# Optimization experiments

Hardware: AMD Instinct MI355X
Metric: run time of the kernel (lower is better)

Reference implementation:

```python
import jax, jax.numpy as jnp
import numpy as np

B, C, H, W = 32, 384, 28, 28
E, HID, K = 4, 384, 2  # HID = hidden_features(1536) // num_experts(4)


def setup_inputs() -> dict:
    key = jax.random.key(0)
    ks = jax.random.split(key, 5)
    x = jax.random.normal(ks[0], (B, C, H, W), jnp.float32)
    gate_w = jax.random.normal(ks[1], (C, E), jnp.float32) * 0.02
    gate_b = jnp.zeros((E,), jnp.float32)
    w1 = jax.random.normal(ks[2], (E, HID, C), jnp.float32) * 0.02
    b1 = jnp.zeros((E, HID), jnp.float32)
    w2 = jax.random.normal(ks[3], (E, C, HID), jnp.float32) * 0.02
    b2 = jnp.zeros((E, C), jnp.float32)
    return {"x": x, "gate_w": gate_w, "gate_b": gate_b,
            "w1": w1, "b1": b1, "w2": w2, "b2": b2}


def reference(x, gate_w, gate_b, w1, b1, w2, b2):
    b, c, h, w = x.shape
    e = gate_b.shape[0]
    # per-token gating: tokens are spatial positions in NHWC order
    x_flat = x.transpose(0, 2, 3, 1).reshape(-1, c)          # [N, C], N = B*H*W
    scores = jax.nn.softmax(x_flat @ gate_w + gate_b, -1)    # [N, E]
    top_v, top_i = jax.lax.top_k(scores, K)                  # [N, K]
    top_w = jax.nn.softmax(top_v, -1)                        # [N, K] renormalized
    # weight map per top-k slot: [K, B, H, W]
    wmap = top_w.T.reshape(K, b, h, w)
    # faithful to torch loop: expert i contributes at slot k iff ANY token routed
    # to it at slot k; the weight applied is the UNMASKED slot-k weight map.
    present = (top_i[:, :, None] == jnp.arange(e)[None, None, :]).any(0)  # [K, E]
    coef = jnp.einsum('ke,kbhw->ebhw', present.astype(x.dtype), wmap)     # [E, B, H, W]
    # dense per-expert 1x1-conv MLP over the FULL tensor (as in the source)
    hdn = jax.nn.relu(jnp.einsum('bchw,edc->ebdhw', x, w1)
                      + b1[:, None, :, None, None])          # [E, B, HID, H, W]
    y = jnp.einsum('ebdhw,eod->ebohw', hdn, w2) + b2[:, None, :, None, None]
    out = jnp.einsum('ebohw,ebhw->bohw', y, coef)            # [B, C, H, W]
    return out
```

## Files before the change

kernel.cpp:

```cpp
#include <hip/hip_runtime.h>
#include <hip/hip_bf16.h>
#include <stdint.h>

#define B_DIM 32
#define C_DIM 384
#define HW_DIM 784
#define E_DIM 4
#define HID_DIM 384
#define NTOK (B_DIM * HW_DIM)
#define NH (E_DIM * HID_DIM)

using short8 = __attribute__((ext_vector_type(8))) short;
using f32x4  = __attribute__((ext_vector_type(4))) float;
typedef unsigned short ushort_t;

__device__ __forceinline__ ushort_t f2bf(float f) {
  __hip_bfloat16 h = __float2bfloat16(f);
  return __builtin_bit_cast(ushort_t, h);
}

__device__ __forceinline__ void gload_lds16(const void* g, void* l) {
  __builtin_amdgcn_global_load_lds(
      (const __attribute__((address_space(1))) unsigned int*)g,
      (__attribute__((address_space(3))) unsigned int*)l, 16, 0, 0);
}

__global__ __launch_bounds__(256) void prep_kernel(
    const float* __restrict__ w1, const float* __restrict__ w2,
    ushort_t* __restrict__ W1b, ushort_t* __restrict__ W2b,
    unsigned int* __restrict__ present) {
  int i = blockIdx.x * 256 + threadIdx.x;
  if (i == 0) *present = 0u;
  if (i < NH * C_DIM) {
    W1b[i] = f2bf(w1[i]);
    int o = i / NH;
    int r = i - o * NH;
    int e = r / HID_DIM;
    int k = r - e * HID_DIM;
    W2b[i] = f2bf(w2[((size_t)e * C_DIM + o) * HID_DIM + k]);
  }
}

__global__ __launch_bounds__(512) void gate_kernel(
    const float* __restrict__ x, const float* __restrict__ gw,
    const float* __restrict__ gb, ushort_t* __restrict__ xb,
    float* __restrict__ topw, unsigned int* __restrict__ present) {
  __shared__ __align__(16) ushort_t lxs[64][392];
  __shared__ float pscore[8][64][4];
  __shared__ unsigned int pmask;
  const int b = blockIdx.x;
  const int p0 = blockIdx.y * 64;
  const int cnt = min(64, HW_DIM - p0);
  const int tid = threadIdx.x;
  const int cg = tid >> 6, tl = tid & 63;
  if (tid == 0) pmask = 0u;
  float a0 = 0.f, a1 = 0.f, a2 = 0.f, a3 = 0.f;
  const bool valid = tl < cnt;
  if (valid) {
    const float* xp = x + (size_t)b * C_DIM * HW_DIM + p0 + tl;
    for (int c = cg; c < C_DIM; c += 8) {
      const float v = xp[(size_t)c * HW_DIM];
      lxs[tl][c] = f2bf(v);
      const float4 g = *(const float4*)&gw[c * 4];
      a0 += v * g.x; a1 += v * g.y; a2 += v * g.z; a3 += v * g.w;
    }
  }
  pscore[cg][tl][0] = a0; pscore[cg][tl][1] = a1;
  pscore[cg][tl][2] = a2; pscore[cg][tl][3] = a3;
  __syncthreads();
  if (cg == 0 && valid) {
    float z[4];
#pragma unroll
    for (int e = 0; e < 4; e++) {
      float s = gb[e];
#pragma unroll
      for (int g8 = 0; g8 < 8; g8++) s += pscore[g8][tl][e];
      z[e] = s;
    }
    const float mx = fmaxf(fmaxf(z[0], z[1]), fmaxf(z[2], z[3]));
    float s[4]; float sum = 0.f;
#pragma unroll
    for (int e = 0; e < 4; e++) { s[e] = __expf(z[e] - mx); sum += s[e]; }
    const float inv = 1.f / sum;
#pragma unroll
    for (int e = 0; e < 4; e++) s[e] *= inv;
    int e0 = 0; float v0 = s[0];
#pragma unroll
    for (int e = 1; e < 4; e++) if (s[e] > v0) { v0 = s[e]; e0 = e; }
    int e1 = -1; float v1 = -1.f;
#pragma unroll
    for (int e = 0; e < 4; e++) if (e != e0 && s[e] > v1) { v1 = s[e]; e1 = e; }
    const float r = __expf(v1 - v0);
    const float w0 = 1.f / (1.f + r);
    const int m = b * HW_DIM + p0 + tl;
    topw[m * 2] = w0;
    topw[m * 2 + 1] = 1.f - w0;
    atomicOr(&pmask, (1u << e0) | (1u << (4 + e1)));
  }
  __syncthreads();
  if (tid == 0) atomicOr(present, pmask);
  const int nchunk = cnt * 48;
  for (int ci = tid; ci < nchunk; ci += 512) {
    const int row = ci / 48, c8 = ci - row * 48;
    short8 v = *(const short8*)&lxs[row][c8 * 8];
    *(short8*)&xb[(size_t)(b * HW_DIM + p0 + row) * C_DIM + c8 * 8] = v;
  }
}

template <int KDIM, int EPI>
__global__ __launch_bounds__(256, 3) void gemm_1b(
    const ushort_t* __restrict__ A, const ushort_t* __restrict__ Bw,
    const float* __restrict__ bias, const float* __restrict__ topw,
    const unsigned int* __restrict__ presentp,
    ushort_t* __restrict__ hOut, float* __restrict__ outp) {
  constexpr int BM = 128, BN = 128, BK = 32;
  constexpr int KT = KDIM / BK;
  constexpr int NTN = (EPI == 0 ? NH / BN : C_DIM / BN);
  constexpr int ASZ = BM * BK;
  __shared__ ushort_t smem[6 * ASZ];

  const int nwg = NTN * (NTOK / BM);
  const int orig = blockIdx.x;
  const int xcd = orig & 7;
  const int qq = nwg >> 3, rr = nwg & 7;
  const int wg = (xcd < rr ? xcd * (qq + 1) : rr * (qq + 1) + (xcd - rr) * qq)
               + (orig >> 3);
  const int mt = wg / NTN, nt = wg % NTN;
  const int m0 = mt * BM, n0 = nt * BN;

  const int tid = threadIdx.x;
  const int lane = tid & 63;
  const int wid = tid >> 6;
  const int wm = wid >> 1, wn = wid & 1;
  const int lanel = lane & 15, laneq = lane >> 4;

  auto stage = [&](int t) {
    const int buf = t % 3;
    ushort_t* dstA = smem + buf * ASZ;
    ushort_t* dstB = smem + 3 * ASZ + buf * ASZ;
    const int kb = t * BK;
#pragma unroll
    for (int li = 0; li < 2; ++li) {
      const int P = (li * 256 + tid) * 16;
      const int row = P >> 6;
      const int cb = (P & 63) ^ (((row >> 1) & 3) << 4);
      gload_lds16(&A[(size_t)(m0 + row) * KDIM + kb + (cb >> 1)],
                  (char*)dstA + P);
    }
#pragma unroll
    for (int li = 0; li < 2; ++li) {
      const int P = (li * 256 + tid) * 16;
      const int row = P >> 6;
      const int cb = (P & 63) ^ (((row >> 1) & 3) << 4);
      gload_lds16(&Bw[(size_t)(n0 + row) * KDIM + kb + (cb >> 1)],
                  (char*)dstB + P);
    }
  };

  f32x4 acc[4][4] = {};
  const int cbr = (laneq * 16) ^ (((lanel >> 1) & 3) << 4);

  stage(0);
  stage(1);
  for (int t = 0; t < KT; ++t) {
    if (t + 1 < KT)
      asm volatile("s_waitcnt vmcnt(4)" ::: "memory");
    else
      asm volatile("s_waitcnt vmcnt(0)" ::: "memory");
    __builtin_amdgcn_sched_barrier(0);
    __builtin_amdgcn_s_barrier();
    __builtin_amdgcn_sched_barrier(0);
    if (t + 2 < KT) stage(t + 2);
    const int buf = t % 3;
    const char* Ab = (const char*)(smem + buf * ASZ) + (wm * 64 + lanel) * 64;
    const char* Bb =
        (const char*)(smem + 3 * ASZ + buf * ASZ) + (wn * 64 + lanel) * 64;
    short8 av[4], bv[4];
#pragma unroll
    for (int i = 0; i < 4; ++i) av[i] = *(const short8*)(Ab + i * 1024 + cbr);
#pragma unroll
    for (int j = 0; j < 4; ++j) bv[j] = *(const short8*)(Bb + j * 1024 + cbr);
    __builtin_amdgcn_s_setprio(1);
#pragma unroll
    for (int i = 0; i < 4; ++i)
#pragma unroll
      for (int j = 0; j < 4; ++j)
        acc[i][j] = __builtin_amdgcn_mfma_f32_16x16x32_bf16(
            av[i], bv[j], acc[i][j], 0, 0, 0);
    __builtin_amdgcn_s_setprio(0);
  }

  const unsigned int pm = *presentp;
  if constexpr (EPI == 0) {
    __syncthreads();
    ushort_t* tr = smem;
    const int e = n0 / HID_DIM;
    const float P0 = (float)((pm >> e) & 1u);
    const float P1 = (float)((pm >> (4 + e)) & 1u);
#pragma unroll
    for (int mi = 0; mi < 4; ++mi) {
      const int r0 = wm * 64 + mi * 16 + laneq * 4;
      const int mg = m0 + r0;
      const float4 t0 = *(const float4*)&topw[mg * 2];
      const float4 t1 = *(const float4*)&topw[mg * 2 + 4];
      const float cj[4] = {P0 * t0.x + P1 * t0.y, P0 * t0.z + P1 * t0.w,
                           P0 * t1.x + P1 * t1.y, P0 * t1.z + P1 * t1.w};
#pragma unroll
      for (int ni = 0; ni < 4; ++ni) {
        const int cl = wn * 64 + ni * 16 + lanel;
        const float bvv = bias[n0 + cl];
#pragma unroll
        for (int j = 0; j < 4; ++j) {
          float v = fmaxf(acc[mi][ni][j] + bvv, 0.f);
          tr[(r0 + j) * 128 + cl] = f2bf(cj[j] * v);
        }
      }
    }
    __syncthreads();
#pragma unroll
    for (int it = 0; it < 8; ++it) {
      const int c = it * 256 + tid;
      const int row = c >> 4, cr = c & 15;
      *(short8*)&hOut[(size_t)(m0 + row) * NH + n0 + cr * 8] =
          *(const short8*)&tr[row * 128 + cr * 8];
    }
  } else {
    float B0[4], B1[4];
#pragma unroll
    for (int ni = 0; ni < 4; ++ni) {
      const int o = n0 + wn * 64 + ni * 16 + lanel;
      float s0 = 0.f, s1 = 0.f;
#pragma unroll
      for (int e2 = 0; e2 < 4; ++e2) {
        const float bb = bias[e2 * C_DIM + o];
        s0 += (float)((pm >> e2) & 1u) * bb;
        s1 += (float)((pm >> (4 + e2)) & 1u) * bb;
      }
      B0[ni] = s0; B1[ni] = s1;
    }
#pragma unroll
    for (int mi = 0; mi < 4; ++mi) {
      const int mg = m0 + wm * 64 + mi * 16 + laneq * 4;
      const float4 t0 = *(const float4*)&topw[mg * 2];
      const float4 t1 = *(const float4*)&topw[mg * 2 + 4];
      const int bb2 = mg / HW_DIM;
      const int p = mg - bb2 * HW_DIM;
#pragma unroll
      for (int ni = 0; ni < 4; ++ni) {
        const int o = n0 + wn * 64 + ni * 16 + lanel;
        float4 v;
        v.x = acc[mi][ni][0] + t0.x * B0[ni] + t0.y * B1[ni];
        v.y = acc[mi][ni][1] + t0.z * B0[ni] + t0.w * B1[ni];
        v.z = acc[mi][ni][2] + t1.x * B0[ni] + t1.y * B1[ni];
        v.w = acc[mi][ni][3] + t1.z * B0[ni] + t1.w * B1[ni];
        *(float4*)&outp[((size_t)bb2 * C_DIM + o) * HW_DIM + p] = v;
      }
    }
  }
}

extern "C" void kernel_launch(void* const* d_in, const int* in_sizes, int n_in,
                              void* d_out, int out_size, void* d_ws, size_t ws_size,
                              hipStream_t stream) {
  const float* x  = (const float*)d_in[0];
  const float* gw = (const float*)d_in[1];
  const float* gb = (const float*)d_in[2];
  const float* w1 = (const float*)d_in[3];
  const float* b1 = (const float*)d_in[4];
  const float* w2 = (const float*)d_in[5];
  const float* b2 = (const float*)d_in[6];
  float* out = (float*)d_out;

  char* ws = (char*)d_ws;
  ushort_t* xb = (ushort_t*)ws;   ws += (size_t)NTOK * C_DIM * 2;
  ushort_t* hdnS = (ushort_t*)ws; ws += (size_t)NTOK * NH * 2;
  ushort_t* W1b = (ushort_t*)ws;  ws += (size_t)NH * C_DIM * 2;
  ushort_t* W2b = (ushort_t*)ws;  ws += (size_t)C_DIM * NH * 2;
  float* topw = (float*)ws;       ws += (size_t)NTOK * 2 * 4;
  unsigned int* present = (unsigned int*)ws;

  prep_kernel<<<dim3((NH * C_DIM) / 256), dim3(256), 0, stream>>>(
      w1, w2, W1b, W2b, present);
  gate_kernel<<<dim3(B_DIM, 13), dim3(512), 0, stream>>>(
      x, gw, gb, xb, topw, present);
  gemm_1b<C_DIM, 0>
      <<<dim3((NTOK / 128) * (NH / 128)), dim3(256), 0, stream>>>(
          xb, W1b, b1, topw, present, hdnS, nullptr);
  gemm_1b<NH, 1>
      <<<dim3((NTOK / 128) * (C_DIM / 128)), dim3(256), 0, stream>>>(
          hdnS, W2b, b2, topw, present, nullptr, out);
}
```

Measured before the change: 121.7 us.

## Load pre-swizzled weight fragments directly into registers, bypassing LDS

```diff
diff --git a/kernel.cpp b/kernel.cpp
--- a/kernel.cpp
+++ b/kernel.cpp
@@ -9,6 +9,7 @@
 #define HID_DIM 384
 #define NTOK (B_DIM * HW_DIM)
 #define NH (E_DIM * HID_DIM)
+#define WSZ 589824
 
 using short8 = __attribute__((ext_vector_type(8))) short;
 using f32x4  = __attribute__((ext_vector_type(4))) float;
@@ -27,17 +28,35 @@
 
 __global__ __launch_bounds__(256) void prep_kernel(
     const float* __restrict__ w1, const float* __restrict__ w2,
-    ushort_t* __restrict__ W1b, ushort_t* __restrict__ W2b,
+    ushort_t* __restrict__ W1f, ushort_t* __restrict__ W2f,
     unsigned int* __restrict__ present) {
   int i = blockIdx.x * 256 + threadIdx.x;
   if (i == 0) *present = 0u;
-  if (i < NH * C_DIM) {
-    W1b[i] = f2bf(w1[i]);
-    int o = i / NH;
-    int r = i - o * NH;
-    int e = r / HID_DIM;
-    int k = r - e * HID_DIM;
-    W2b[i] = f2bf(w2[((size_t)e * C_DIM + o) * HID_DIM + k]);
+  if (i >= WSZ) return;
+  {
+    int r = i;
+    const int nt = r / 49152; r -= nt * 49152;
+    const int ks = r / 4096;  r -= ks * 4096;
+    const int wn = r >> 11;
+    const int ni = (r >> 9) & 3;
+    const int ln = (r >> 3) & 63;
+    const int tt = r & 7;
+    const int row = nt * 128 + wn * 64 + ni * 16 + (ln & 15);
+    const int c = ks * 32 + (ln >> 4) * 8 + tt;
+    W1f[i] = f2bf(w1[(size_t)row * C_DIM + c]);
+  }
+  {
+    int r = i;
+    const int nt = r / 196608; r -= nt * 196608;
+    const int ks = r / 4096;   r -= ks * 4096;
+    const int wn = r >> 11;
+    const int ni = (r >> 9) & 3;
+    const int ln = (r >> 3) & 63;
+    const int tt = r & 7;
+    const int o = nt * 128 + wn * 64 + ni * 16 + (ln & 15);
+    const int kg = ks * 32 + (ln >> 4) * 8 + tt;
+    const int e = kg / HID_DIM, d = kg - e * HID_DIM;
+    W2f[i] = f2bf(w2[((size_t)e * C_DIM + o) * HID_DIM + d]);
   }
 }
 
@@ -108,8 +127,8 @@
 }
 
 template <int KDIM, int EPI>
-__global__ __launch_bounds__(256, 3) void gemm_1b(
-    const ushort_t* __restrict__ A, const ushort_t* __restrict__ Bw,
+__global__ __launch_bounds__(256, 3) void gemm_bg(
+    const ushort_t* __restrict__ A, const ushort_t* __restrict__ Wf,
     const float* __restrict__ bias, const float* __restrict__ topw,
     const unsigned int* __restrict__ presentp,
     ushort_t* __restrict__ hOut, float* __restrict__ outp) {
@@ -117,7 +136,7 @@
   constexpr int KT = KDIM / BK;
   constexpr int NTN = (EPI == 0 ? NH / BN : C_DIM / BN);
   constexpr int ASZ = BM * BK;
-  __shared__ ushort_t smem[6 * ASZ];
+  __shared__ ushort_t smem[3 * ASZ];
 
   const int nwg = NTN * (NTOK / BM);
   const int orig = blockIdx.x;
@@ -134,10 +153,10 @@
   const int wm = wid >> 1, wn = wid & 1;
   const int lanel = lane & 15, laneq = lane >> 4;
 
+  const ushort_t* wbase = Wf + (size_t)nt * KT * 4096 + wn * 2048 + lane * 8;
+
   auto stage = [&](int t) {
-    const int buf = t % 3;
-    ushort_t* dstA = smem + buf * ASZ;
-    ushort_t* dstB = smem + 3 * ASZ + buf * ASZ;
+    ushort_t* dstA = smem + (t % 3) * ASZ;
     const int kb = t * BK;
 #pragma unroll
     for (int li = 0; li < 2; ++li) {
@@ -147,47 +166,57 @@
       gload_lds16(&A[(size_t)(m0 + row) * KDIM + kb + (cb >> 1)],
                   (char*)dstA + P);
     }
-#pragma unroll
-    for (int li = 0; li < 2; ++li) {
-      const int P = (li * 256 + tid) * 16;
-      const int row = P >> 6;
-      const int cb = (P & 63) ^ (((row >> 1) & 3) << 4);
-      gload_lds16(&Bw[(size_t)(n0 + row) * KDIM + kb + (cb >> 1)],
-                  (char*)dstB + P);
-    }
+  };
+
+  auto loadB = [&](int t, short8* bv) {
+    const ushort_t* p = wbase + (size_t)t * 4096;
+    asm volatile(
+        "global_load_dwordx4 %0, %4, off\n\t"
+        "global_load_dwordx4 %1, %4, off offset:1024\n\t"
+        "global_load_dwordx4 %2, %4, off offset:2048\n\t"
+        "global_load_dwordx4 %3, %4, off offset:3072"
+        : "=&v"(bv[0]), "=&v"(bv[1]), "=&v"(bv[2]), "=&v"(bv[3])
+        : "v"(p)
+        : "memory");
   };
 
   f32x4 acc[4][4] = {};
   const int cbr = (laneq * 16) ^ (((lanel >> 1) & 3) << 4);
 
-  stage(0);
-  stage(1);
-  for (int t = 0; t < KT; ++t) {
+  short8 bvA[4], bvB[4];
+
+  auto step = [&](int t, short8* cur, short8* nxt) {
     if (t + 1 < KT)
-      asm volatile("s_waitcnt vmcnt(4)" ::: "memory");
+      asm volatile("s_waitcnt vmcnt(2)" ::: "memory");
     else
       asm volatile("s_waitcnt vmcnt(0)" ::: "memory");
     __builtin_amdgcn_sched_barrier(0);
     __builtin_amdgcn_s_barrier();
     __builtin_amdgcn_sched_barrier(0);
+    if (t + 1 < KT) loadB(t + 1, nxt);
+    __builtin_amdgcn_sched_barrier(0);
     if (t + 2 < KT) stage(t + 2);
-    const int buf = t % 3;
-    const char* Ab = (const char*)(smem + buf * ASZ) + (wm * 64 + lanel) * 64;
-    const char* Bb =
-        (const char*)(smem + 3 * ASZ + buf * ASZ) + (wn * 64 + lanel) * 64;
-    short8 av[4], bv[4];
+    const char* Ab =
+        (const char*)(smem + (t % 3) * ASZ) + (wm * 64 + lanel) * 64;
+    short8 av[4];
 #pragma unroll
     for (int i = 0; i < 4; ++i) av[i] = *(const short8*)(Ab + i * 1024 + cbr);
-#pragma unroll
-    for (int j = 0; j < 4; ++j) bv[j] = *(const short8*)(Bb + j * 1024 + cbr);
     __builtin_amdgcn_s_setprio(1);
 #pragma unroll
     for (int i = 0; i < 4; ++i)
 #pragma unroll
       for (int j = 0; j < 4; ++j)
         acc[i][j] = __builtin_amdgcn_mfma_f32_16x16x32_bf16(
-            av[i], bv[j], acc[i][j], 0, 0, 0);
+            av[i], cur[j], acc[i][j], 0, 0, 0);
     __builtin_amdgcn_s_setprio(0);
+  };
+
+  stage(0);
+  loadB(0, bvA);
+  stage(1);
+  for (int t = 0; t < KT; t += 2) {
+    step(t, bvA, bvB);
+    step(t + 1, bvB, bvA);
   }
 
   const unsigned int pm = *presentp;
@@ -198,31 +227,37 @@
     const float P0 = (float)((pm >> e) & 1u);
     const float P1 = (float)((pm >> (4 + e)) & 1u);
 #pragma unroll
-    for (int mi = 0; mi < 4; ++mi) {
-      const int r0 = wm * 64 + mi * 16 + laneq * 4;
-      const int mg = m0 + r0;
-      const float4 t0 = *(const float4*)&topw[mg * 2];
-      const float4 t1 = *(const float4*)&topw[mg * 2 + 4];
-      const float cj[4] = {P0 * t0.x + P1 * t0.y, P0 * t0.z + P1 * t0.w,
-                           P0 * t1.x + P1 * t1.y, P0 * t1.z + P1 * t1.w};
-#pragma unroll
-      for (int ni = 0; ni < 4; ++ni) {
-        const int cl = wn * 64 + ni * 16 + lanel;
-        const float bvv = bias[n0 + cl];
-#pragma unroll
-        for (int j = 0; j < 4; ++j) {
-          float v = fmaxf(acc[mi][ni][j] + bvv, 0.f);
-          tr[(r0 + j) * 128 + cl] = f2bf(cj[j] * v);
+    for (int s = 0; s < 2; ++s) {
+      if (wm == s) {
+#pragma unroll
+        for (int mi = 0; mi < 4; ++mi) {
+          const int r0 = mi * 16 + laneq * 4;
+          const int mg = m0 + s * 64 + r0;
+          const float4 t0 = *(const float4*)&topw[mg * 2];
+          const float4 t1 = *(const float4*)&topw[mg * 2 + 4];
+          const float cj[4] = {P0 * t0.x + P1 * t0.y, P0 * t0.z + P1 * t0.w,
+                               P0 * t1.x + P1 * t1.y, P0 * t1.z + P1 * t1.w};
+#pragma unroll
+          for (int ni = 0; ni < 4; ++ni) {
+            const int cl = wn * 64 + ni * 16 + lanel;
+            const float bvv = bias[n0 + cl];
+#pragma unroll
+            for (int j = 0; j < 4; ++j) {
+              float v = fmaxf(acc[mi][ni][j] + bvv, 0.f);
+              tr[(r0 + j) * 128 + cl] = f2bf(cj[j] * v);
+            }
+          }
         }
       }
-    }
-    __syncthreads();
-#pragma unroll
-    for (int it = 0; it < 8; ++it) {
-      const int c = it * 256 + tid;
-      const int row = c >> 4, cr = c & 15;
-      *(short8*)&hOut[(size_t)(m0 + row) * NH + n0 + cr * 8] =
-          *(const short8*)&tr[row * 128 + cr * 8];
+      __syncthreads();
+#pragma unroll
+      for (int it = 0; it < 4; ++it) {
+        const int c = it * 256 + tid;
+        const int row = c >> 4, cr = c & 15;
+        *(short8*)&hOut[(size_t)(m0 + s * 64 + row) * NH + n0 + cr * 8] =
+            *(const short8*)&tr[row * 128 + cr * 8];
+      }
+      __syncthreads();
     }
   } else {
     float B0[4], B1[4];
@@ -274,19 +309,19 @@
   char* ws = (char*)d_ws;
   ushort_t* xb = (ushort_t*)ws;   ws += (size_t)NTOK * C_DIM * 2;
   ushort_t* hdnS = (ushort_t*)ws; ws += (size_t)NTOK * NH * 2;
-  ushort_t* W1b = (ushort_t*)ws;  ws += (size_t)NH * C_DIM * 2;
-  ushort_t* W2b = (ushort_t*)ws;  ws += (size_t)C_DIM * NH * 2;
+  ushort_t* W1f = (ushort_t*)ws;  ws += (size_t)WSZ * 2;
+  ushort_t* W2f = (ushort_t*)ws;  ws += (size_t)WSZ * 2;
   float* topw = (float*)ws;       ws += (size_t)NTOK * 2 * 4;
   unsigned int* present = (unsigned int*)ws;
 
-  prep_kernel<<<dim3((NH * C_DIM) / 256), dim3(256), 0, stream>>>(
-      w1, w2, W1b, W2b, present);
+  prep_kernel<<<dim3(WSZ / 256), dim3(256), 0, stream>>>(
+      w1, w2, W1f, W2f, present);
   gate_kernel<<<dim3(B_DIM, 13), dim3(512), 0, stream>>>(
       x, gw, gb, xb, topw, present);
-  gemm_1b<C_DIM, 0>
+  gemm_bg<C_DIM, 0>
       <<<dim3((NTOK / 128) * (NH / 128)), dim3(256), 0, stream>>>(
-          xb, W1b, b1, topw, present, hdnS, nullptr);
-  gemm_1b<NH, 1>
+          xb, W1f, b1, topw, present, hdnS, nullptr);
+  gemm_bg<NH, 1>
       <<<dim3((NTOK / 128) * (C_DIM / 128)), dim3(256), 0, stream>>>(
-          hdnS, W2b, b2, topw, present, nullptr, out);
-}
+          hdnS, W2f, b2, topw, present, nullptr, out);
+}
```

New measurement: 120.1 us. Within noise of the previous version (-1.3%).
